# Kernel tuning notes

Measured on AMD Instinct MI355X. Metric: run time of the kernel, lower is better.

## Reference

```python
import jax, jax.numpy as jnp
import numpy as np

N = 8192          # number of nodes
IN_F = 256        # in_features
OUT_F = 128       # out_features
ALPHA = 0.2       # LeakyReLU negative slope


def setup_inputs() -> dict:
    key = jax.random.key(0)
    k1, k2, k3, k4 = jax.random.split(key, 4)
    h = jax.random.normal(k1, (N, IN_F), dtype=jnp.float32)
    adj = jax.random.randint(k2, (N, N), 0, 2, dtype=jnp.int32)  # dense 0/1 adjacency mask
    W = (jax.random.normal(k3, (IN_F, OUT_F), dtype=jnp.float32) * 0.05)   # W.weight^T
    a = (jax.random.normal(k4, (2 * OUT_F,), dtype=jnp.float32) * 0.05)    # a.weight flattened
    return {"h": h, "adj": adj, "W": W, "a": a}


def reference(h, adj, W, a):
    # Wh = self.W(h): [N, OUT_F]
    Wh = h @ W
    # Original builds an [N, N, 2F] concat tensor then projects with 'a'.
    # Equivalent math: e[i, j] = leaky_relu(Wh[i]@a1 + Wh[j]@a2)
    a1, a2 = a[:OUT_F], a[OUT_F:]
    src = Wh @ a1                                     # [N] per-source score
    dst = Wh @ a2                                     # [N] per-target score
    e = jax.nn.leaky_relu(src[:, None] + dst[None, :], negative_slope=ALPHA)  # [N, N]
    # masked softmax over neighbors (dim=1); adj==0 -> -inf
    e = jnp.where(adj == 0, -jnp.inf, e)
    attention = jax.nn.softmax(e, axis=1)             # [N, N]
    # dropout p=0 in eval-mode reference -> identity
    h_prime = attention @ Wh                          # [N, OUT_F]
    return jax.nn.elu(h_prime)                        # concat=True -> ELU
```

## Files before the change

kernel.cpp:

```cpp
#include <hip/hip_runtime.h>
#include <math.h>

#define N 8192
#define IN_F 256
#define OUT_F 128
#define ALPHA 0.2f
#define JS 8
#define NSTEP 32
#define MW (N / 32)

typedef _Float16 f16;
typedef __attribute__((ext_vector_type(4))) float f32x4;
typedef __attribute__((ext_vector_type(8))) _Float16 f16x8;
typedef __attribute__((ext_vector_type(4))) _Float16 f16x4;

__global__ __launch_bounds__(256) void k_prep(const float* __restrict__ W,
                                              f16* __restrict__ WT) {
    int idx = blockIdx.x * 256 + threadIdx.x;
    int f = idx >> 8;
    int k = idx & 255;
    WT[idx] = (f16)W[k * OUT_F + f];
}

__global__ __launch_bounds__(256) void k_pack(const int* __restrict__ adj,
                                              unsigned* __restrict__ M) {
    const int t = threadIdx.x;
    const int l = t & 63;
    const size_t tot = (size_t)N * N / 4;
    const size_t stride = (size_t)gridDim.x * 256;
    size_t idx = (size_t)blockIdx.x * 256 + t;
    const int4* ap = (const int4*)adj;
    for (; idx < tot; idx += stride) {
        int4 v = ap[idx];
        unsigned m = (v.x ? 1u : 0u) | (v.y ? 2u : 0u) | (v.z ? 4u : 0u) | (v.w ? 8u : 0u);
        m |= __shfl_down(m, 1) << 4;
        m |= __shfl_down(m, 2) << 8;
        m |= __shfl_down(m, 4) << 16;
        if ((l & 7) == 0) M[idx >> 3] = m;
    }
}

#define HS 280
__global__ __launch_bounds__(256) void k_wh(const float* __restrict__ h,
                                            const f16* __restrict__ WT,
                                            const float* __restrict__ a,
                                            f16* __restrict__ WhT,
                                            float* __restrict__ src,
                                            float* __restrict__ dst) {
    __shared__ __align__(16) f16 hA[32][HS];
    __shared__ __align__(16) f16 outT[128][40];
    __shared__ float sred[4][32], dred[4][32];

    const int t = threadIdx.x;
    const int i0 = blockIdx.x * 32;
    const int wv = t >> 6, l = t & 63, ln = l & 15, lq = l >> 4;

    {
        const float4* hg = (const float4*)(h + (size_t)i0 * IN_F);
#pragma unroll
        for (int it = 0; it < 8; ++it) {
            int idx = t + it * 256;
            int r = idx >> 6;
            int c4 = (idx & 63) * 4;
            float4 v = hg[idx];
            f16x4 p = { (f16)v.x, (f16)v.y, (f16)v.z, (f16)v.w };
            *(f16x4*)&hA[r][c4] = p;
        }
    }
    __syncthreads();

    f32x4 acc00 = {0.f,0.f,0.f,0.f}, acc01 = {0.f,0.f,0.f,0.f};
    f32x4 acc10 = {0.f,0.f,0.f,0.f}, acc11 = {0.f,0.f,0.f,0.f};
    const int f0 = 32 * wv;

#pragma unroll
    for (int ks = 0; ks < 8; ++ks) {
        const int k0 = 32 * ks + 8 * lq;
        f16x8 a0 = *(const f16x8*)&hA[ln][k0];
        f16x8 a1 = *(const f16x8*)&hA[16 + ln][k0];
        f16x8 b0 = *(const f16x8*)(WT + (size_t)(f0 + ln) * IN_F + k0);
        f16x8 b1 = *(const f16x8*)(WT + (size_t)(f0 + 16 + ln) * IN_F + k0);
        acc00 = __builtin_amdgcn_mfma_f32_16x16x32_f16(a0, b0, acc00, 0, 0, 0);
        acc01 = __builtin_amdgcn_mfma_f32_16x16x32_f16(a0, b1, acc01, 0, 0, 0);
        acc10 = __builtin_amdgcn_mfma_f32_16x16x32_f16(a1, b0, acc10, 0, 0, 0);
        acc11 = __builtin_amdgcn_mfma_f32_16x16x32_f16(a1, b1, acc11, 0, 0, 0);
    }

    const float a1c0 = a[f0 + ln],      a2c0 = a[128 + f0 + ln];
    const float a1c1 = a[f0 + 16 + ln], a2c1 = a[128 + f0 + 16 + ln];
    float sp[8], dp[8];
#pragma unroll
    for (int i = 0; i < 8; ++i) { sp[i] = 0.f; dp[i] = 0.f; }

#pragma unroll
    for (int hh = 0; hh < 2; ++hh) {
        f32x4 v0 = hh ? acc10 : acc00;
        f32x4 v1 = hh ? acc11 : acc01;
        f16x4 p0, p1;
#pragma unroll
        for (int rg = 0; rg < 4; ++rg) {
            sp[hh * 4 + rg] += v0[rg] * a1c0 + v1[rg] * a1c1;
            dp[hh * 4 + rg] += v0[rg] * a2c0 + v1[rg] * a2c1;
            p0[rg] = (f16)v0[rg];
            p1[rg] = (f16)v1[rg];
        }
        *(f16x4*)&outT[f0 + ln][16 * hh + 4 * lq] = p0;
        *(f16x4*)&outT[f0 + 16 + ln][16 * hh + 4 * lq] = p1;
    }
#pragma unroll
    for (int i = 0; i < 8; ++i) {
        float s = sp[i], d = dp[i];
        s += __shfl_down(s, 8, 16); d += __shfl_down(d, 8, 16);
        s += __shfl_down(s, 4, 16); d += __shfl_down(d, 4, 16);
        s += __shfl_down(s, 2, 16); d += __shfl_down(d, 2, 16);
        s += __shfl_down(s, 1, 16); d += __shfl_down(d, 1, 16);
        if (ln == 0) {
            int row = 16 * (i >> 2) + 4 * lq + (i & 3);
            sred[wv][row] = s;
            dred[wv][row] = d;
        }
    }
    __syncthreads();
    if (t < 32) {
        src[i0 + t] = sred[0][t] + sred[1][t] + sred[2][t] + sred[3][t];
        dst[i0 + t] = dred[0][t] + dred[1][t] + dred[2][t] + dred[3][t];
    }
    {
        const int col = t & 127, g = t >> 7;
        const int ct = i0 >> 7, jo = i0 & 127;
        f16x8 q0 = *(const f16x8*)&outT[col][16 * g];
        f16x8 q1 = *(const f16x8*)&outT[col][16 * g + 8];
        f16* dstp = WhT + (size_t)ct * (128 * 128) + (size_t)col * 128 + jo + 16 * g;
        *(f16x8*)(dstp) = q0;
        *(f16x8*)(dstp + 8) = q1;
    }
}

__global__ __launch_bounds__(256, 2) void k_attn(const unsigned* __restrict__ M,
                                                 const f16* __restrict__ WhT,
                                                 const float* __restrict__ src,
                                                 const float* __restrict__ dst,
                                                 float* __restrict__ p_part,
                                                 float* __restrict__ l_part) {
    const int t = threadIdx.x;
    const int wv = t >> 6, l = t & 63, ln = l & 15, lq = l >> 4;
    const int i0 = (blockIdx.x * 4 + wv) * 32;
    const int jq = blockIdx.y;
    const int jbase = jq * (N / JS);

    const float src0 = src[i0 + ln];
    const float src1 = src[i0 + 16 + ln];
    const float c0 = fabsf(src0) + 4.0f;
    const float c1 = fabsf(src1) + 4.0f;
    float lp0 = 0.f, lp1 = 0.f;

    f32x4 acc0[8], acc1[8];
#pragma unroll
    for (int ft = 0; ft < 8; ++ft) {
        acc0[ft] = (f32x4){0.f,0.f,0.f,0.f};
        acc1[ft] = (f32x4){0.f,0.f,0.f,0.f};
    }

    const unsigned* Mr0 = M + (size_t)(i0 + ln) * MW + jq * (NSTEP);
    const unsigned* Mr1 = Mr0 + (size_t)16 * MW;
    const float* drow = dst + jbase + 8 * lq;
    const f16* Bb = WhT + (size_t)(jq * 8) * (128 * 128) + (size_t)ln * 128 + 8 * lq;

    float4 pd[2][2];
    auto dissue = [&](int s, int p) {
        const int off = 32 * (s & (NSTEP - 1));
        pd[p][0] = *(const float4*)(drow + off);
        pd[p][1] = *(const float4*)(drow + off + 4);
    };
    f16x8 bfb[2][8];
    auto bissue = [&](int s) {
        const int ss = s & (NSTEP - 1);
        const f16* bp = Bb + (ss >> 2) * (128 * 128) + (ss & 3) * 32;
#pragma unroll
        for (int ft = 0; ft < 8; ++ft)
            bfb[s & 1][ft] = *(const f16x8*)(bp + ft * (16 * 128));
    };

    uint4 m0c = *(const uint4*)Mr0;
    uint4 m1c = *(const uint4*)Mr1;
    dissue(0, 0);
    dissue(1, 1);
    bissue(0);

    for (int g = 0; g < 8; ++g) {
        uint4 m0n, m1n;
        if (g < 7) {
            m0n = *(const uint4*)(Mr0 + 4 * (g + 1));
            m1n = *(const uint4*)(Mr1 + 4 * (g + 1));
        }
#pragma unroll
        for (int s4 = 0; s4 < 4; ++s4) {
            const int s = 4 * g + s4;
            const int p = s & 1;
            const float4 d0 = pd[p][0], d1 = pd[p][1];
            dissue(s + 2, p);
            bissue(s + 1);
            const unsigned b0 = (((const unsigned*)&m0c)[s4] >> (8 * lq)) & 0xffu;
            const unsigned b1 = (((const unsigned*)&m1c)[s4] >> (8 * lq)) & 0xffu;
            const float* df0 = (const float*)&d0;
            const float* df1 = (const float*)&d1;
            f16x8 af0, af1;
#pragma unroll
            for (int k = 0; k < 8; ++k) {
                const float dv = (k < 4) ? df0[k] : df1[k - 4];
                float e0 = src0 + dv;
                float w0 = (b0 >> k) & 1u ? __expf(fmaxf(e0, ALPHA * e0) - c0) : 0.f;
                lp0 += w0; af0[k] = (f16)w0;
                float e1 = src1 + dv;
                float w1 = (b1 >> k) & 1u ? __expf(fmaxf(e1, ALPHA * e1) - c1) : 0.f;
                lp1 += w1; af1[k] = (f16)w1;
            }
#pragma unroll
            for (int ft = 0; ft < 8; ++ft) {
                f16x8 bf = bfb[p][ft];
                acc0[ft] = __builtin_amdgcn_mfma_f32_16x16x32_f16(af0, bf, acc0[ft], 0, 0, 0);
                acc1[ft] = __builtin_amdgcn_mfma_f32_16x16x32_f16(af1, bf, acc1[ft], 0, 0, 0);
            }
        }
        if (g < 7) { m0c = m0n; m1c = m1n; }
    }

    lp0 += __shfl_down(lp0, 32); lp0 += __shfl_down(lp0, 16);
    lp1 += __shfl_down(lp1, 32); lp1 += __shfl_down(lp1, 16);
    if (l < 16) {
        l_part[(size_t)jq * N + i0 + l] = lp0;
        l_part[(size_t)jq * N + i0 + 16 + l] = lp1;
    }

    float* pb = p_part + (size_t)jq * N * OUT_F;
#pragma unroll
    for (int ft = 0; ft < 8; ++ft) {
#pragma unroll
        for (int rg = 0; rg < 4; ++rg) {
            pb[(size_t)(i0 + 4 * lq + rg) * OUT_F + 16 * ft + ln] = acc0[ft][rg];
            pb[(size_t)(i0 + 16 + 4 * lq + rg) * OUT_F + 16 * ft + ln] = acc1[ft][rg];
        }
    }
}

__global__ __launch_bounds__(256) void k_comb(const float* __restrict__ p_part,
                                              const float* __restrict__ l_part,
                                              float* __restrict__ out) {
    const int idx4 = blockIdx.x * 256 + threadIdx.x;
    const int row = idx4 >> 5;
    const float4* pp = (const float4*)p_part;
    float4 p = pp[idx4];
    float lsum = l_part[row];
#pragma unroll
    for (int q = 1; q < JS; ++q) {
        float4 v = pp[(size_t)q * (N * OUT_F / 4) + idx4];
        p.x += v.x; p.y += v.y; p.z += v.z; p.w += v.w;
        lsum += l_part[(size_t)q * N + row];
    }
    float inv = 1.0f / lsum;
    float4 r;
    r.x = p.x * inv; r.x = r.x > 0.f ? r.x : expm1f(r.x);
    r.y = p.y * inv; r.y = r.y > 0.f ? r.y : expm1f(r.y);
    r.z = p.z * inv; r.z = r.z > 0.f ? r.z : expm1f(r.z);
    r.w = p.w * inv; r.w = r.w > 0.f ? r.w : expm1f(r.w);
    ((float4*)out)[idx4] = r;
}

extern "C" void kernel_launch(void* const* d_in, const int* in_sizes, int n_in,
                              void* d_out, int out_size, void* d_ws, size_t ws_size,
                              hipStream_t stream) {
    const float* h   = (const float*)d_in[0];
    const int*   adj = (const int*)d_in[1];
    const float* W   = (const float*)d_in[2];
    const float* a   = (const float*)d_in[3];
    float* out = (float*)d_out;

    char* ws = (char*)d_ws;
    f16*      WT     = (f16*)ws;        ws += 64 * 1024;
    f16*      WhT    = (f16*)ws;        ws += 2 * 1024 * 1024;
    float*    src    = (float*)ws;      ws += N * sizeof(float);
    float*    dst    = (float*)ws;      ws += N * sizeof(float);
    float*    l_part = (float*)ws;      ws += (size_t)JS * N * sizeof(float);
    unsigned* M      = (unsigned*)ws;   ws += (size_t)N * MW * sizeof(unsigned);
    float*    p_part = (float*)ws;

    k_pack<<<2048, 256, 0, stream>>>(adj, M);
    k_prep<<<128, 256, 0, stream>>>(W, WT);
    k_wh<<<N / 32, 256, 0, stream>>>(h, WT, a, WhT, src, dst);
    dim3 agrid(N / 128, JS);
    k_attn<<<agrid, 256, 0, stream>>>(M, WhT, src, dst, p_part, l_part);
    k_comb<<<N * OUT_F / 4 / 256, 256, 0, stream>>>(p_part, l_part, out);
}
```

Measured before the change: 488.3 us.

## Pre-pack Wh into MFMA fragment layout and drop B double-buffering in attention

k_wh now writes Wh as fragment-ordered tiles, so each lane's B operand for a step and feature tile sits in a contiguous 16-byte slot and a wave reads a contiguous 1 KB block. k_attn loads B fragments directly at each step instead of prefetching them one step ahead into a double buffer, and the dst prefetch is cut to one step ahead. Launch bounds change from two blocks per CU to one, which frees registers but may lower occupancy and expose global-load latency now that B is no longer prefetched.

```diff
diff --git a/kernel.cpp b/kernel.cpp
--- a/kernel.cpp
+++ b/kernel.cpp
@@ -44,7 +44,7 @@
 __global__ __launch_bounds__(256) void k_wh(const float* __restrict__ h,
                                             const f16* __restrict__ WT,
                                             const float* __restrict__ a,
-                                            f16* __restrict__ WhT,
+                                            f16* __restrict__ Bpack,
                                             float* __restrict__ src,
                                             float* __restrict__ dst) {
     __shared__ __align__(16) f16 hA[32][HS];
@@ -126,18 +126,19 @@
         dst[i0 + t] = dred[0][t] + dred[1][t] + dred[2][t] + dred[3][t];
     }
     {
-        const int col = t & 127, g = t >> 7;
-        const int ct = i0 >> 7, jo = i0 & 127;
-        f16x8 q0 = *(const f16x8*)&outT[col][16 * g];
-        f16x8 q1 = *(const f16x8*)&outT[col][16 * g + 8];
-        f16* dstp = WhT + (size_t)ct * (128 * 128) + (size_t)col * 128 + jo + 16 * g;
-        *(f16x8*)(dstp) = q0;
-        *(f16x8*)(dstp + 8) = q1;
-    }
-}
-
-__global__ __launch_bounds__(256, 2) void k_attn(const unsigned* __restrict__ M,
-                                                 const f16* __restrict__ WhT,
+        const size_t gs = (size_t)(i0 >> 5);
+        const int ft0 = t >> 6;
+#pragma unroll
+        for (int hh = 0; hh < 2; ++hh) {
+            const int ft = ft0 + 4 * hh;
+            f16x8 v = *(const f16x8*)&outT[16 * ft + ln][8 * lq];
+            *(f16x8*)(Bpack + (gs * 8 + ft) * 512 + l * 8) = v;
+        }
+    }
+}
+
+__global__ __launch_bounds__(256, 1) void k_attn(const unsigned* __restrict__ M,
+                                                 const f16* __restrict__ Bpack,
                                                  const float* __restrict__ src,
                                                  const float* __restrict__ dst,
                                                  float* __restrict__ p_part,
@@ -146,7 +147,6 @@
     const int wv = t >> 6, l = t & 63, ln = l & 15, lq = l >> 4;
     const int i0 = (blockIdx.x * 4 + wv) * 32;
     const int jq = blockIdx.y;
-    const int jbase = jq * (N / JS);
 
     const float src0 = src[i0 + ln];
     const float src1 = src[i0 + 16 + ln];
@@ -161,31 +161,15 @@
         acc1[ft] = (f32x4){0.f,0.f,0.f,0.f};
     }
 
-    const unsigned* Mr0 = M + (size_t)(i0 + ln) * MW + jq * (NSTEP);
+    const unsigned* Mr0 = M + (size_t)(i0 + ln) * MW + jq * NSTEP;
     const unsigned* Mr1 = Mr0 + (size_t)16 * MW;
-    const float* drow = dst + jbase + 8 * lq;
-    const f16* Bb = WhT + (size_t)(jq * 8) * (128 * 128) + (size_t)ln * 128 + 8 * lq;
-
-    float4 pd[2][2];
-    auto dissue = [&](int s, int p) {
-        const int off = 32 * (s & (NSTEP - 1));
-        pd[p][0] = *(const float4*)(drow + off);
-        pd[p][1] = *(const float4*)(drow + off + 4);
-    };
-    f16x8 bfb[2][8];
-    auto bissue = [&](int s) {
-        const int ss = s & (NSTEP - 1);
-        const f16* bp = Bb + (ss >> 2) * (128 * 128) + (ss & 3) * 32;
-#pragma unroll
-        for (int ft = 0; ft < 8; ++ft)
-            bfb[s & 1][ft] = *(const f16x8*)(bp + ft * (16 * 128));
-    };
+    const float* drow = dst + jq * (N / JS) + 8 * lq;
+    const f16* Bb = Bpack + (size_t)(jq * NSTEP) * 8 * 512 + l * 8;
 
     uint4 m0c = *(const uint4*)Mr0;
     uint4 m1c = *(const uint4*)Mr1;
-    dissue(0, 0);
-    dissue(1, 1);
-    bissue(0);
+    float4 cd0 = *(const float4*)(drow);
+    float4 cd1 = *(const float4*)(drow + 4);
 
     for (int g = 0; g < 8; ++g) {
         uint4 m0n, m1n;
@@ -196,10 +180,17 @@
 #pragma unroll
         for (int s4 = 0; s4 < 4; ++s4) {
             const int s = 4 * g + s4;
-            const int p = s & 1;
-            const float4 d0 = pd[p][0], d1 = pd[p][1];
-            dissue(s + 2, p);
-            bissue(s + 1);
+            const f16* bp = Bb + (size_t)s * (8 * 512);
+            f16x8 bf[8];
+#pragma unroll
+            for (int ft = 0; ft < 8; ++ft)
+                bf[ft] = *(const f16x8*)(bp + ft * 512);
+            const float4 d0 = cd0, d1 = cd1;
+            {
+                const int off = 32 * ((s + 1) & (NSTEP - 1));
+                cd0 = *(const float4*)(drow + off);
+                cd1 = *(const float4*)(drow + off + 4);
+            }
             const unsigned b0 = (((const unsigned*)&m0c)[s4] >> (8 * lq)) & 0xffu;
             const unsigned b1 = (((const unsigned*)&m1c)[s4] >> (8 * lq)) & 0xffu;
             const float* df0 = (const float*)&d0;
@@ -217,9 +208,8 @@
             }
 #pragma unroll
             for (int ft = 0; ft < 8; ++ft) {
-                f16x8 bf = bfb[p][ft];
-                acc0[ft] = __builtin_amdgcn_mfma_f32_16x16x32_f16(af0, bf, acc0[ft], 0, 0, 0);
-                acc1[ft] = __builtin_amdgcn_mfma_f32_16x16x32_f16(af1, bf, acc1[ft], 0, 0, 0);
+                acc0[ft] = __builtin_amdgcn_mfma_f32_16x16x32_f16(af0, bf[ft], acc0[ft], 0, 0, 0);
+                acc1[ft] = __builtin_amdgcn_mfma_f32_16x16x32_f16(af1, bf[ft], acc1[ft], 0, 0, 0);
             }
         }
         if (g < 7) { m0c = m0n; m1c = m1n; }
@@ -277,7 +267,7 @@
 
     char* ws = (char*)d_ws;
     f16*      WT     = (f16*)ws;        ws += 64 * 1024;
-    f16*      WhT    = (f16*)ws;        ws += 2 * 1024 * 1024;
+    f16*      Bpack  = (f16*)ws;        ws += 2 * 1024 * 1024;
     float*    src    = (float*)ws;      ws += N * sizeof(float);
     float*    dst    = (float*)ws;      ws += N * sizeof(float);
     float*    l_part = (float*)ws;      ws += (size_t)JS * N * sizeof(float);
@@ -286,8 +276,8 @@
 
     k_pack<<<2048, 256, 0, stream>>>(adj, M);
     k_prep<<<128, 256, 0, stream>>>(W, WT);
-    k_wh<<<N / 32, 256, 0, stream>>>(h, WT, a, WhT, src, dst);
+    k_wh<<<N / 32, 256, 0, stream>>>(h, WT, a, Bpack, src, dst);
     dim3 agrid(N / 128, JS);
-    k_attn<<<agrid, 256, 0, stream>>>(M, WhT, src, dst, p_part, l_part);
+    k_attn<<<agrid, 256, 0, stream>>>(M, Bpack, src, dst, p_part, l_part);
     k_comb<<<N * OUT_F / 4 / 256, 256, 0, stream>>>(p_part, l_part, out);
 }
```

Result: faster. 419.0 us (-14.2%).
